# Performance work log

Hardware: AMD Instinct MI355X
Metric: run time of the kernel (lower is better)

The kernel has to match this reference:

```python
import jax, jax.numpy as jnp
import numpy as np

SEQ, BATCH = 64, 32
X_DIM, Z_DIM, Y_DIM, H_DIM, N_LAYERS = 32, 128, 16, 128, 3
PARAM_SHAPES = [(H_DIM, X_DIM), (H_DIM,), (H_DIM, H_DIM), (H_DIM,), (Y_DIM, H_DIM), (Y_DIM,)]
SIZES = [int(np.prod(s)) for s in PARAM_SHAPES]
NBLOCKS = [(s + Z_DIM - 1) // Z_DIM for s in SIZES]
OFFSETS = np.cumsum([0] + NBLOCKS)          # static block offsets per param tensor
TOTAL_NB = int(OFFSETS[-1])                  # 179 fastfood blocks total


def fwht(x):
    """Unnormalized Walsh-Hadamard transform over last axis (power-of-2 dim)."""
    d = x.shape[-1]
    h = 2
    while h <= d:
        x = x.reshape(x.shape[:-1] + (d // h, h))
        a, b = x[..., : h // 2], x[..., h // 2:]
        x = jnp.concatenate([a + b, a - b], axis=-1).reshape(x.shape[:-2] + (d,))
        h *= 2
    return x


def setup_inputs() -> dict:
    key = jax.random.key(0)
    ks = jax.random.split(key, 16)
    inp = {
        "x": jax.random.normal(ks[0], (SEQ, BATCH, X_DIM), jnp.float32),
        "z": jax.random.normal(ks[1], (SEQ, BATCH, Z_DIM), jnp.float32),
    }
    # base MLP parameters (nn.Linear default init: U(-1/sqrt(fan_in), 1/sqrt(fan_in)))
    for i in range(N_LAYERS):
        w_shape, b_shape = PARAM_SHAPES[2 * i], PARAM_SHAPES[2 * i + 1]
        s = 1.0 / np.sqrt(w_shape[1])
        inp[f"W0_{i}"] = jax.random.uniform(ks[2 + 2 * i], w_shape, jnp.float32, -s, s)
        inp[f"b0_{i}"] = jax.random.uniform(ks[3 + 2 * i], b_shape, jnp.float32, -s, s)
    # FastFood params stacked over all blocks of all param tensors
    inp["ffB"] = jnp.where(jax.random.bernoulli(ks[10], 0.5, (TOTAL_NB, Z_DIM)), 1.0, -1.0).astype(jnp.float32)
    inp["ffG"] = jax.random.normal(ks[11], (TOTAL_NB, Z_DIM), jnp.float32)
    inp["ffS"] = jax.random.normal(ks[12], (TOTAL_NB, Z_DIM), jnp.float32) * 0.01
    inp["ffP"] = jnp.argsort(jax.random.uniform(ks[13], (TOTAL_NB, Z_DIM)), axis=-1).astype(jnp.int32)
    return inp


def reference(x, z, W0_0, b0_0, W0_1, b0_1, W0_2, b0_2, ffB, ffG, ffS, ffP):
    N = SEQ * BATCH
    zf = z.reshape(N, Z_DIM)
    # FastFood upsample for all blocks at once: S * H * G * Pi * H * B * z
    v = ffB[None] * zf[:, None, :]                       # (N, NB, d)
    v = fwht(v)
    rows = jnp.arange(TOTAL_NB)[:, None]
    v = v[:, rows, ffP]                                  # per-block permutation
    v = ffG[None] * v
    v = fwht(v)
    v = ffS[None] * v / Z_DIM                            # (N, NB, d)

    Ws, bs = [W0_0, W0_1, W0_2], [b0_0, b0_1, b0_2]
    h = x
    for i in range(N_LAYERS):
        wi, bi = 2 * i, 2 * i + 1
        wd = v[:, OFFSETS[wi]:OFFSETS[wi + 1], :].reshape(N, -1)[:, :SIZES[wi]]
        wd = wd.reshape(SEQ, BATCH, *PARAM_SHAPES[wi])
        bd = v[:, OFFSETS[bi]:OFFSETS[bi + 1], :].reshape(N, -1)[:, :SIZES[bi]]
        bd = bd.reshape(SEQ, BATCH, *PARAM_SHAPES[bi])
        w = Ws[i][None, None] + wd                       # (seq, batch, out, in)
        b = bs[i][None, None] + bd                       # (seq, batch, out)
        h = jnp.einsum('sbi,sbji->sbj', h, w) + b
        if i < N_LAYERS - 1:
            h = jax.nn.relu(h)
    return h
```

## Files before the change

### kernel.cpp

```cpp
#include <hip/hip_runtime.h>
#include <hip/hip_fp16.h>


#define NTOK 2048

typedef _Float16 f16x8 __attribute__((ext_vector_type(8)));
typedef _Float16 f16x4 __attribute__((ext_vector_type(4)));
typedef float f32x4 __attribute__((ext_vector_type(4)));
typedef unsigned int u32;

__device__ __forceinline__ float2 pk_add(float2 a, float2 b) {
  float2 d;
  asm("v_pk_add_f32 %0, %1, %2" : "=v"(d) : "v"(a), "v"(b));
  return d;
}
__device__ __forceinline__ float2 pk_sub(float2 a, float2 b) {
  float2 d;
  asm("v_pk_add_f32 %0, %1, %2 neg_lo:[0,1] neg_hi:[0,1]" : "=v"(d) : "v"(a), "v"(b));
  return d;
}

__device__ __forceinline__ void fwht128p(float2 w[64]) {
#pragma unroll
  for (int m = 0; m < 64; m++) {
    float a = w[m].x, b = w[m].y;
    w[m].x = a + b; w[m].y = a - b;
  }
#pragma unroll
  for (int sig = 1; sig < 64; sig <<= 1) {
#pragma unroll
    for (int m = 0; m < 64; m++) {
      if ((m & sig) == 0) {
        float2 a = w[m], b = w[m + sig];
        w[m] = pk_add(a, b);
        w[m + sig] = pk_sub(a, b);
      }
    }
  }
}

__global__ __launch_bounds__(128) void km(
    const float* __restrict__ ffB, const float* __restrict__ ffG,
    const float* __restrict__ ffS, const int* __restrict__ ffP,
    _Float16* __restrict__ M) {
  __shared__ _Float16 T[128 * 128];
  __shared__ float sG[128], sS[128];
  __shared__ int sP[128];
  const int tid = threadIdx.x;
  const int j = blockIdx.x;
  sG[tid] = ffG[(size_t)j * 128 + tid];
  sS[tid] = ffS[(size_t)j * 128 + tid];
  sP[tid] = ffP[(size_t)j * 128 + tid];
  __syncthreads();
  const float Bc = ffB[(size_t)j * 128 + tid];
  float2 w[64];
#pragma unroll
  for (int m = 0; m < 64; m++) {
    int p0 = sP[2 * m], p1 = sP[2 * m + 1];
    float s0 = (__popc(p0 & tid) & 1) ? -Bc : Bc;
    float s1 = (__popc(p1 & tid) & 1) ? -Bc : Bc;
    w[m].x = sG[2 * m] * s0;
    w[m].y = sG[2 * m + 1] * s1;
  }
  fwht128p(w);
#pragma unroll
  for (int m = 0; m < 64; m++) {
    T[(2 * m) * 128 + tid] = (_Float16)(w[m].x * sS[2 * m] * 0.0078125f);
    T[(2 * m + 1) * 128 + tid] = (_Float16)(w[m].y * sS[2 * m + 1] * 0.0078125f);
  }
  __syncthreads();
  const u32* Ts = (const u32*)T;
  u32* Mo = (u32*)(M + (size_t)j * 16384);
#pragma unroll 4
  for (int i = 0; i < 64; i++) Mo[i * 128 + tid] = Ts[i * 128 + tid];
}

template <int MODE, int JB>
__global__ __launch_bounds__(256, 2) void gf(
    const _Float16* __restrict__ M, const float* __restrict__ z,
    int j0, int jbias,
    const float* __restrict__ xin,
    const float* __restrict__ hin,
    const float* __restrict__ Wp, const float* __restrict__ bp,
    float* __restrict__ outp) {
  __shared__ _Float16 Asm[128 * 136];
  __shared__ _Float16 Bsm[128 * 136];
  __shared__ _Float16 pM[4 * 136];
  __shared__ float pW[128];
  const int tid = threadIdx.x;
  const int lane = tid & 63, wv = tid >> 6;
  const int ln = lane & 15, g = lane >> 4;
  const int strip = blockIdx.x;
  const int tl0 = wv * 32 + ln;
  const int tg0 = strip * 128 + tl0;

  {
    const float4* zg = (const float4*)z + (size_t)(strip * 128) * 32;
#pragma unroll
    for (int i = 0; i < 16; i++) {
      int F = i * 256 + tid;
      int t = F >> 5, q = F & 31;
      float4 f = zg[(size_t)t * 32 + q];
      __half2 hlo = __floats2half2_rn(f.x, f.y);
      __half2 hhi = __floats2half2_rn(f.z, f.w);
      uint2 u = make_uint2(*(u32*)&hlo, *(u32*)&hhi);
      *(uint2*)(&Bsm[t * 136 + q * 4]) = u;
    }
  }

  float4 xa[2][2];
  if constexpr (MODE == 0) {
#pragma unroll
    for (int tt = 0; tt < 2; tt++) {
      const float* xr = xin + (size_t)(tg0 + tt * 16) * 32;
      xa[tt][0] = *(const float4*)(xr + g * 4);
      xa[tt][1] = *(const float4*)(xr + 16 + g * 4);
    }
  }

#pragma unroll 1
  for (int jj = 0; jj < JB; jj++) {
    const int row = blockIdx.y * JB + jj;
    const int j = j0 + row;

    {
      const uint4* Mg = (const uint4*)(M + (size_t)j * 16384);
#pragma unroll
      for (int i = 0; i < 8; i++) {
        int F = i * 256 + tid;
        int v = F >> 4, c = F & 15;
        *(uint4*)(&Asm[v * 136 + c * 8]) = Mg[F];
      }
    }
    if constexpr (MODE == 0) {
      {
        const u32* src = (const u32*)(M + (size_t)jbias * 16384 + (size_t)(4 * j) * 128);
        int rr = tid >> 6, uu = tid & 63;
        *(u32*)(&pM[rr * 136 + uu * 2]) = src[rr * 64 + uu];
      }
      if (tid < 128) pW[tid] = Wp[(size_t)(4 * j) * 32 + tid];
    } else {
      if (tid < 64) {
        const u32* src = (const u32*)(M + (size_t)jbias * 16384 + (size_t)row * 128);
        *(u32*)(&pM[tid * 2]) = src[tid];
      }
      if (tid < 128) pW[tid] = Wp[(size_t)row * 128 + tid];
    }
    __syncthreads();

    f32x4 acc[8][2];
#pragma unroll
    for (int vt = 0; vt < 8; vt++)
#pragma unroll
      for (int tt = 0; tt < 2; tt++) {
        f32x4 zf = {0.f, 0.f, 0.f, 0.f};
        acc[vt][tt] = zf;
      }
#pragma unroll
    for (int ks = 0; ks < 4; ks++) {
      f16x8 af[8], bf[2];
#pragma unroll
      for (int vt = 0; vt < 8; vt++)
        af[vt] = *(const f16x8*)(&Asm[(vt * 16 + ln) * 136 + ks * 32 + g * 8]);
#pragma unroll
      for (int tt = 0; tt < 2; tt++)
        bf[tt] = *(const f16x8*)(&Bsm[(wv * 32 + tt * 16 + ln) * 136 + ks * 32 + g * 8]);
#pragma unroll
      for (int vt = 0; vt < 8; vt++)
#pragma unroll
        for (int tt = 0; tt < 2; tt++)
          acc[vt][tt] = __builtin_amdgcn_mfma_f32_16x16x32_f16(af[vt], bf[tt],
                                                               acc[vt][tt], 0, 0, 0);
    }

    if constexpr (MODE == 0) {
      float pw[2][4] = {{0, 0, 0, 0}, {0, 0, 0, 0}};
      float pb[2][4] = {{0, 0, 0, 0}, {0, 0, 0, 0}};
#pragma unroll
      for (int vt = 0; vt < 8; vt++) {
        const int rho = vt >> 1;
        const float4 w4 = *(const float4*)&pW[rho * 32 + (vt & 1) * 16 + g * 4];
#pragma unroll
        for (int r = 0; r < 4; r++) {
          const float* xp0 = &xa[0][vt & 1].x;
          const float* xp1 = &xa[1][vt & 1].x;
          const float* wp4 = &w4.x;
          pw[0][rho] += acc[vt][0][r] * xp0[r];
          pw[1][rho] += acc[vt][1][r] * xp1[r];
          pb[0][rho] += wp4[r] * xp0[r];
          pb[1][rho] += wp4[r] * xp1[r];
        }
      }
#pragma unroll
      for (int tt = 0; tt < 2; tt++) {
#pragma unroll
        for (int uu = 0; uu < 8; uu++) {
          int u0 = g * 32 + uu * 4;
          f16x4 zh = *(const f16x4*)(&Bsm[(tl0 + tt * 16) * 136 + u0]);
          float zf0 = (float)zh[0], zf1 = (float)zh[1], zf2 = (float)zh[2], zf3 = (float)zh[3];
#pragma unroll
          for (int rho = 0; rho < 4; rho++) {
            f16x4 mh = *(const f16x4*)(&pM[rho * 136 + u0]);
            pw[tt][rho] += (float)mh[0] * zf0 + (float)mh[1] * zf1 +
                           (float)mh[2] * zf2 + (float)mh[3] * zf3;
          }
        }
      }
#pragma unroll
      for (int tt = 0; tt < 2; tt++)
#pragma unroll
        for (int rho = 0; rho < 4; rho++) {
          pw[tt][rho] += __shfl_xor(pw[tt][rho], 16);
          pw[tt][rho] += __shfl_xor(pw[tt][rho], 32);
          pb[tt][rho] += __shfl_xor(pb[tt][rho], 16);
          pb[tt][rho] += __shfl_xor(pb[tt][rho], 32);
        }
      if (g == 0) {
#pragma unroll
        for (int tt = 0; tt < 2; tt++) {
          float4 o;
          float* op = &o.x;
#pragma unroll
          for (int rho = 0; rho < 4; rho++)
            op[rho] = fmaxf(pb[tt][rho] + pw[tt][rho] + bp[4 * j + rho], 0.f);
          *(float4*)(outp + (size_t)(tg0 + tt * 16) * 128 + 4 * j) = o;
        }
      }
    } else {
      float pw0 = 0.f, pw1 = 0.f, pb0 = 0.f, pb1 = 0.f;
#pragma unroll
      for (int vt = 0; vt < 8; vt++) {
        const int v0 = vt * 16 + g * 4;
        const float4 w4 = *(const float4*)&pW[v0];
        const float4 h0 = *(const float4*)(hin + (size_t)tg0 * 128 + v0);
        const float4 h1v = *(const float4*)(hin + (size_t)(tg0 + 16) * 128 + v0);
        const float* wp4 = &w4.x;
        const float* hp0 = &h0.x;
        const float* hp1 = &h1v.x;
#pragma unroll
        for (int r = 0; r < 4; r++) {
          pw0 += acc[vt][0][r] * hp0[r];
          pw1 += acc[vt][1][r] * hp1[r];
          pb0 += wp4[r] * hp0[r];
          pb1 += wp4[r] * hp1[r];
        }
      }
#pragma unroll
      for (int uu = 0; uu < 8; uu++) {
        int u0 = g * 32 + uu * 4;
        f16x4 mh = *(const f16x4*)(&pM[u0]);
        f16x4 z0 = *(const f16x4*)(&Bsm[tl0 * 136 + u0]);
        f16x4 z1 = *(const f16x4*)(&Bsm[(tl0 + 16) * 136 + u0]);
#pragma unroll
        for (int e = 0; e < 4; e++) {
          pw0 += (float)mh[e] * (float)z0[e];
          pw1 += (float)mh[e] * (float)z1[e];
        }
      }
      pw0 += __shfl_xor(pw0, 16); pw0 += __shfl_xor(pw0, 32);
      pw1 += __shfl_xor(pw1, 16); pw1 += __shfl_xor(pw1, 32);
      pb0 += __shfl_xor(pb0, 16); pb0 += __shfl_xor(pb0, 32);
      pb1 += __shfl_xor(pb1, 16); pb1 += __shfl_xor(pb1, 32);
      if (g == 0) {
        float bias = bp[row];
        float v0 = pb0 + pw0 + bias;
        float v1 = pb1 + pw1 + bias;
        if constexpr (MODE == 1) {
          outp[(size_t)tg0 * 128 + row] = fmaxf(v0, 0.f);
          outp[(size_t)(tg0 + 16) * 128 + row] = fmaxf(v1, 0.f);
        } else {
          outp[(size_t)tg0 * 16 + row] = v0;
          outp[(size_t)(tg0 + 16) * 16 + row] = v1;
        }
      }
    }
    __syncthreads();
  }
}

extern "C" void kernel_launch(void* const* d_in, const int* in_sizes, int n_in,
                              void* d_out, int out_size, void* d_ws, size_t ws_size,
                              hipStream_t stream) {
  const float* x  = (const float*)d_in[0];
  const float* z  = (const float*)d_in[1];
  const float* W0 = (const float*)d_in[2];
  const float* b0 = (const float*)d_in[3];
  const float* W1 = (const float*)d_in[4];
  const float* b1 = (const float*)d_in[5];
  const float* W2 = (const float*)d_in[6];
  const float* b2 = (const float*)d_in[7];
  const float* fB = (const float*)d_in[8];
  const float* fG = (const float*)d_in[9];
  const float* fS = (const float*)d_in[10];
  const int*   fP = (const int*)d_in[11];
  float* out = (float*)d_out;
  (void)ws_size;

  char* p = (char*)d_ws;
  _Float16* Mbuf = (_Float16*)p; p += (size_t)179 * 16384 * 2;
  float* h1 = (float*)p;         p += (size_t)NTOK * 128 * 4;
  float* h2 = (float*)p;         p += (size_t)NTOK * 128 * 4;

  km<<<dim3(179), 128, 0, stream>>>(fB, fG, fS, fP, Mbuf);
  gf<0, 2><<<dim3(16, 16), 256, 0, stream>>>(Mbuf, z, 0, 32, x, nullptr, W0, b0, h1);
  gf<1, 2><<<dim3(16, 64), 256, 0, stream>>>(Mbuf, z, 33, 161, nullptr, h1, W1, b1, h2);
  gf<2, 2><<<dim3(16, 8), 256, 0, stream>>>(Mbuf, z, 162, 178, nullptr, h2, W2, b2, out);
}
```

Measured before the change: 126.1 us.

## Fuse fastfood and three layer kernels into one cooperative persistent kernel

```diff
diff --git a/kernel.cpp b/kernel.cpp
--- a/kernel.cpp
+++ b/kernel.cpp
@@ -1,13 +1,19 @@
 #include <hip/hip_runtime.h>
 #include <hip/hip_fp16.h>
+#include <hip/hip_cooperative_groups.h>
+
+namespace cg = cooperative_groups;
 
 
 #define NTOK 2048
 
 typedef _Float16 f16x8 __attribute__((ext_vector_type(8)));
-typedef _Float16 f16x4 __attribute__((ext_vector_type(4)));
 typedef float f32x4 __attribute__((ext_vector_type(4)));
 typedef unsigned int u32;
+
+struct ShM { _Float16 T[128 * 128]; float sG[128]; float sS[128]; int sP[128]; };
+struct ShG { _Float16 Asm[128 * 136]; _Float16 pM[4 * 136]; float pW[128]; };
+union Sh { ShM m; ShG g; };
 
 __device__ __forceinline__ float2 pk_add(float2 a, float2 b) {
   float2 d;
@@ -39,74 +45,68 @@
   }
 }
 
-__global__ __launch_bounds__(128) void km(
-    const float* __restrict__ ffB, const float* __restrict__ ffG,
-    const float* __restrict__ ffS, const int* __restrict__ ffP,
+__device__ __forceinline__ void km_body(ShM& m, int tid, int j,
+    const float* __restrict__ fB, const float* __restrict__ fG,
+    const float* __restrict__ fS, const int* __restrict__ fP,
     _Float16* __restrict__ M) {
-  __shared__ _Float16 T[128 * 128];
-  __shared__ float sG[128], sS[128];
-  __shared__ int sP[128];
-  const int tid = threadIdx.x;
-  const int j = blockIdx.x;
-  sG[tid] = ffG[(size_t)j * 128 + tid];
-  sS[tid] = ffS[(size_t)j * 128 + tid];
-  sP[tid] = ffP[(size_t)j * 128 + tid];
+  if (tid < 128) {
+    m.sG[tid] = fG[(size_t)j * 128 + tid];
+    m.sS[tid] = fS[(size_t)j * 128 + tid];
+    m.sP[tid] = fP[(size_t)j * 128 + tid];
+  }
   __syncthreads();
-  const float Bc = ffB[(size_t)j * 128 + tid];
-  float2 w[64];
-#pragma unroll
-  for (int m = 0; m < 64; m++) {
-    int p0 = sP[2 * m], p1 = sP[2 * m + 1];
-    float s0 = (__popc(p0 & tid) & 1) ? -Bc : Bc;
-    float s1 = (__popc(p1 & tid) & 1) ? -Bc : Bc;
-    w[m].x = sG[2 * m] * s0;
-    w[m].y = sG[2 * m + 1] * s1;
-  }
-  fwht128p(w);
-#pragma unroll
-  for (int m = 0; m < 64; m++) {
-    T[(2 * m) * 128 + tid] = (_Float16)(w[m].x * sS[2 * m] * 0.0078125f);
-    T[(2 * m + 1) * 128 + tid] = (_Float16)(w[m].y * sS[2 * m + 1] * 0.0078125f);
+  if (tid < 128) {
+    const float Bc = fB[(size_t)j * 128 + tid];
+    float2 w[64];
+#pragma unroll
+    for (int q = 0; q < 64; q++) {
+      int p0 = m.sP[2 * q], p1 = m.sP[2 * q + 1];
+      float s0 = (__popc(p0 & tid) & 1) ? -Bc : Bc;
+      float s1 = (__popc(p1 & tid) & 1) ? -Bc : Bc;
+      w[q].x = m.sG[2 * q] * s0;
+      w[q].y = m.sG[2 * q + 1] * s1;
+    }
+    fwht128p(w);
+#pragma unroll
+    for (int q = 0; q < 64; q++) {
+      m.T[(2 * q) * 128 + tid] = (_Float16)(w[q].x * m.sS[2 * q] * 0.0078125f);
+      m.T[(2 * q + 1) * 128 + tid] = (_Float16)(w[q].y * m.sS[2 * q + 1] * 0.0078125f);
+    }
   }
   __syncthreads();
-  const u32* Ts = (const u32*)T;
-  u32* Mo = (u32*)(M + (size_t)j * 16384);
+  if (tid < 128) {
+    const u32* Ts = (const u32*)m.T;
+    u32* Mo = (u32*)(M + (size_t)j * 16384);
 #pragma unroll 4
-  for (int i = 0; i < 64; i++) Mo[i * 128 + tid] = Ts[i * 128 + tid];
+    for (int i = 0; i < 64; i++) Mo[i * 128 + tid] = Ts[i * 128 + tid];
+  }
+}
+
+__device__ __forceinline__ void load_bf(f16x8 (&bf)[2][4],
+    const float* __restrict__ z, int tg0, int g) {
+#pragma unroll
+  for (int tt = 0; tt < 2; tt++)
+#pragma unroll
+    for (int ks = 0; ks < 4; ks++) {
+      const float* zp = z + (size_t)(tg0 + tt * 16) * 128 + ks * 32 + g * 8;
+      float4 a = *(const float4*)zp;
+      float4 b = *(const float4*)(zp + 4);
+      f16x8 v;
+      v[0] = (_Float16)a.x; v[1] = (_Float16)a.y; v[2] = (_Float16)a.z; v[3] = (_Float16)a.w;
+      v[4] = (_Float16)b.x; v[5] = (_Float16)b.y; v[6] = (_Float16)b.z; v[7] = (_Float16)b.w;
+      bf[tt][ks] = v;
+    }
 }
 
 template <int MODE, int JB>
-__global__ __launch_bounds__(256, 2) void gf(
-    const _Float16* __restrict__ M, const float* __restrict__ z,
-    int j0, int jbias,
-    const float* __restrict__ xin,
-    const float* __restrict__ hin,
+__device__ __forceinline__ void gf_phase(ShG& S, const f16x8 (&bf)[2][4],
+    const _Float16* __restrict__ M, int j0, int row0, int jbias,
+    const float* __restrict__ xin, const float* __restrict__ hin,
     const float* __restrict__ Wp, const float* __restrict__ bp,
-    float* __restrict__ outp) {
-  __shared__ _Float16 Asm[128 * 136];
-  __shared__ _Float16 Bsm[128 * 136];
-  __shared__ _Float16 pM[4 * 136];
-  __shared__ float pW[128];
-  const int tid = threadIdx.x;
+    float* __restrict__ outp, int tid, int strip) {
   const int lane = tid & 63, wv = tid >> 6;
   const int ln = lane & 15, g = lane >> 4;
-  const int strip = blockIdx.x;
-  const int tl0 = wv * 32 + ln;
-  const int tg0 = strip * 128 + tl0;
-
-  {
-    const float4* zg = (const float4*)z + (size_t)(strip * 128) * 32;
-#pragma unroll
-    for (int i = 0; i < 16; i++) {
-      int F = i * 256 + tid;
-      int t = F >> 5, q = F & 31;
-      float4 f = zg[(size_t)t * 32 + q];
-      __half2 hlo = __floats2half2_rn(f.x, f.y);
-      __half2 hhi = __floats2half2_rn(f.z, f.w);
-      uint2 u = make_uint2(*(u32*)&hlo, *(u32*)&hhi);
-      *(uint2*)(&Bsm[t * 136 + q * 4]) = u;
-    }
-  }
+  const int tg0 = strip * 128 + wv * 32 + ln;
 
   float4 xa[2][2];
   if constexpr (MODE == 0) {
@@ -120,31 +120,28 @@
 
 #pragma unroll 1
   for (int jj = 0; jj < JB; jj++) {
-    const int row = blockIdx.y * JB + jj;
-    const int j = j0 + row;
+    const int j = j0 + jj;
+    const int row = row0 + jj;
 
     {
       const uint4* Mg = (const uint4*)(M + (size_t)j * 16384);
 #pragma unroll
       for (int i = 0; i < 8; i++) {
         int F = i * 256 + tid;
-        int v = F >> 4, c = F & 15;
-        *(uint4*)(&Asm[v * 136 + c * 8]) = Mg[F];
+        *(uint4*)(&S.Asm[(F >> 4) * 136 + (F & 15) * 8]) = Mg[F];
       }
     }
     if constexpr (MODE == 0) {
-      {
-        const u32* src = (const u32*)(M + (size_t)jbias * 16384 + (size_t)(4 * j) * 128);
-        int rr = tid >> 6, uu = tid & 63;
-        *(u32*)(&pM[rr * 136 + uu * 2]) = src[rr * 64 + uu];
-      }
-      if (tid < 128) pW[tid] = Wp[(size_t)(4 * j) * 32 + tid];
+      const u32* src = (const u32*)(M + (size_t)jbias * 16384 + (size_t)(4 * j) * 128);
+      int rr = tid >> 6, uu = tid & 63;
+      *(u32*)(&S.pM[rr * 136 + uu * 2]) = src[rr * 64 + uu];
+      if (tid < 128) S.pW[tid] = Wp[(size_t)(4 * j) * 32 + tid];
     } else {
       if (tid < 64) {
         const u32* src = (const u32*)(M + (size_t)jbias * 16384 + (size_t)row * 128);
-        *(u32*)(&pM[tid * 2]) = src[tid];
-      }
-      if (tid < 128) pW[tid] = Wp[(size_t)row * 128 + tid];
+        *(u32*)(&S.pM[tid * 2]) = src[tid];
+      }
+      if (tid < 128) S.pW[tid] = Wp[(size_t)row * 128 + tid];
     }
     __syncthreads();
 
@@ -158,18 +155,15 @@
       }
 #pragma unroll
     for (int ks = 0; ks < 4; ks++) {
-      f16x8 af[8], bf[2];
+      f16x8 af[8];
 #pragma unroll
       for (int vt = 0; vt < 8; vt++)
-        af[vt] = *(const f16x8*)(&Asm[(vt * 16 + ln) * 136 + ks * 32 + g * 8]);
-#pragma unroll
-      for (int tt = 0; tt < 2; tt++)
-        bf[tt] = *(const f16x8*)(&Bsm[(wv * 32 + tt * 16 + ln) * 136 + ks * 32 + g * 8]);
+        af[vt] = *(const f16x8*)(&S.Asm[(vt * 16 + ln) * 136 + ks * 32 + g * 8]);
 #pragma unroll
       for (int vt = 0; vt < 8; vt++)
 #pragma unroll
         for (int tt = 0; tt < 2; tt++)
-          acc[vt][tt] = __builtin_amdgcn_mfma_f32_16x16x32_f16(af[vt], bf[tt],
+          acc[vt][tt] = __builtin_amdgcn_mfma_f32_16x16x32_f16(af[vt], bf[tt][ks],
                                                                acc[vt][tt], 0, 0, 0);
     }
 
@@ -179,7 +173,7 @@
 #pragma unroll
       for (int vt = 0; vt < 8; vt++) {
         const int rho = vt >> 1;
-        const float4 w4 = *(const float4*)&pW[rho * 32 + (vt & 1) * 16 + g * 4];
+        const float4 w4 = *(const float4*)&S.pW[rho * 32 + (vt & 1) * 16 + g * 4];
 #pragma unroll
         for (int r = 0; r < 4; r++) {
           const float* xp0 = &xa[0][vt & 1].x;
@@ -192,20 +186,18 @@
         }
       }
 #pragma unroll
-      for (int tt = 0; tt < 2; tt++) {
-#pragma unroll
-        for (int uu = 0; uu < 8; uu++) {
-          int u0 = g * 32 + uu * 4;
-          f16x4 zh = *(const f16x4*)(&Bsm[(tl0 + tt * 16) * 136 + u0]);
-          float zf0 = (float)zh[0], zf1 = (float)zh[1], zf2 = (float)zh[2], zf3 = (float)zh[3];
+      for (int tt = 0; tt < 2; tt++)
+#pragma unroll
+        for (int ks = 0; ks < 4; ks++) {
+          f16x8 zb = bf[tt][ks];
 #pragma unroll
           for (int rho = 0; rho < 4; rho++) {
-            f16x4 mh = *(const f16x4*)(&pM[rho * 136 + u0]);
-            pw[tt][rho] += (float)mh[0] * zf0 + (float)mh[1] * zf1 +
-                           (float)mh[2] * zf2 + (float)mh[3] * zf3;
+            f16x8 mh = *(const f16x8*)(&S.pM[rho * 136 + ks * 32 + g * 8]);
+#pragma unroll
+            for (int e = 0; e < 8; e++)
+              pw[tt][rho] += (float)mh[e] * (float)zb[e];
           }
         }
-      }
 #pragma unroll
       for (int tt = 0; tt < 2; tt++)
 #pragma unroll
@@ -231,7 +223,7 @@
 #pragma unroll
       for (int vt = 0; vt < 8; vt++) {
         const int v0 = vt * 16 + g * 4;
-        const float4 w4 = *(const float4*)&pW[v0];
+        const float4 w4 = *(const float4*)&S.pW[v0];
         const float4 h0 = *(const float4*)(hin + (size_t)tg0 * 128 + v0);
         const float4 h1v = *(const float4*)(hin + (size_t)(tg0 + 16) * 128 + v0);
         const float* wp4 = &w4.x;
@@ -246,13 +238,11 @@
         }
       }
 #pragma unroll
-      for (int uu = 0; uu < 8; uu++) {
-        int u0 = g * 32 + uu * 4;
-        f16x4 mh = *(const f16x4*)(&pM[u0]);
-        f16x4 z0 = *(const f16x4*)(&Bsm[tl0 * 136 + u0]);
-        f16x4 z1 = *(const f16x4*)(&Bsm[(tl0 + 16) * 136 + u0]);
-#pragma unroll
-        for (int e = 0; e < 4; e++) {
+      for (int ks = 0; ks < 4; ks++) {
+        f16x8 mh = *(const f16x8*)(&S.pM[ks * 32 + g * 8]);
+        f16x8 z0 = bf[0][ks], z1 = bf[1][ks];
+#pragma unroll
+        for (int e = 0; e < 8; e++) {
           pw0 += (float)mh[e] * (float)z0[e];
           pw1 += (float)mh[e] * (float)z1[e];
         }
@@ -276,6 +266,74 @@
     }
     __syncthreads();
   }
+}
+
+__global__ __launch_bounds__(256) void fused(
+    _Float16* __restrict__ M,
+    const float* __restrict__ z, const float* __restrict__ x,
+    const float* __restrict__ W0, const float* __restrict__ b0,
+    const float* __restrict__ W1, const float* __restrict__ b1,
+    const float* __restrict__ W2, const float* __restrict__ b2,
+    const float* __restrict__ fB, const float* __restrict__ fG,
+    const float* __restrict__ fS, const int* __restrict__ fP,
+    float* __restrict__ h1, float* __restrict__ h2, float* __restrict__ out) {
+  __shared__ Sh sh;
+  const int tid = threadIdx.x;
+  const int bid = blockIdx.x;
+  cg::grid_group grid = cg::this_grid();
+  const int strip = bid >> 4;
+  const int lane = tid & 63, wv = tid >> 6, ln = lane & 15, g = lane >> 4;
+  const int tg0 = strip * 128 + wv * 32 + ln;
+
+  f16x8 bf[2][4];
+  load_bf(bf, z, tg0, g);
+
+  if (bid < 179) km_body(sh.m, tid, bid, fB, fG, fS, fP, M);
+  __threadfence();
+  grid.sync();
+  __threadfence();
+
+  gf_phase<0, 2>(sh.g, bf, M, (bid & 15) * 2, (bid & 15) * 2, 32, x, nullptr,
+                 W0, b0, h1, tid, strip);
+  __threadfence();
+  grid.sync();
+  __threadfence();
+
+  gf_phase<1, 8>(sh.g, bf, M, 33 + (bid & 15) * 8, (bid & 15) * 8, 161, nullptr,
+                 h1, W1, b1, h2, tid, strip);
+  __threadfence();
+  grid.sync();
+  __threadfence();
+
+  gf_phase<2, 1>(sh.g, bf, M, 162 + (bid & 15), (bid & 15), 178, nullptr,
+                 h2, W2, b2, out, tid, strip);
+}
+
+__global__ __launch_bounds__(256) void km_k(
+    const float* __restrict__ fB, const float* __restrict__ fG,
+    const float* __restrict__ fS, const int* __restrict__ fP,
+    _Float16* __restrict__ M) {
+  __shared__ ShM m;
+  km_body(m, threadIdx.x, blockIdx.x, fB, fG, fS, fP, M);
+}
+
+template <int MODE, int JB>
+__global__ __launch_bounds__(256) void gf_k(
+    const _Float16* __restrict__ M, const float* __restrict__ z,
+    const float* __restrict__ xin, const float* __restrict__ hin,
+    const float* __restrict__ Wp, const float* __restrict__ bp,
+    float* __restrict__ outp) {
+  __shared__ ShG S;
+  const int tid = threadIdx.x;
+  const int strip = blockIdx.x;
+  const int lane = tid & 63, wv = tid >> 6, ln = lane & 15, g = lane >> 4;
+  const int tg0 = strip * 128 + wv * 32 + ln;
+  f16x8 bf[2][4];
+  load_bf(bf, z, tg0, g);
+  const int row0 = blockIdx.y * JB;
+  const int j0 = (MODE == 0) ? row0 : (MODE == 1 ? 33 + row0 : 162 + row0);
+  const int jbias = (MODE == 0) ? 32 : (MODE == 1 ? 161 : 178);
+  gf_phase<MODE, JB>(S, bf, M, j0, row0, jbias, xin, hin, Wp, bp, outp, tid, strip);
 }
 
 extern "C" void kernel_launch(void* const* d_in, const int* in_sizes, int n_in,
@@ -301,8 +359,14 @@
   float* h1 = (float*)p;         p += (size_t)NTOK * 128 * 4;
   float* h2 = (float*)p;         p += (size_t)NTOK * 128 * 4;
 
-  km<<<dim3(179), 128, 0, stream>>>(fB, fG, fS, fP, Mbuf);
-  gf<0, 2><<<dim3(16, 16), 256, 0, stream>>>(Mbuf, z, 0, 32, x, nullptr, W0, b0, h1);
-  gf<1, 2><<<dim3(16, 64), 256, 0, stream>>>(Mbuf, z, 33, 161, nullptr, h1, W1, b1, h2);
-  gf<2, 2><<<dim3(16, 8), 256, 0, stream>>>(Mbuf, z, 162, 178, nullptr, h2, W2, b2, out);
-}
+  void* args[] = {&Mbuf, &z, &x, &W0, &b0, &W1, &b1, &W2, &b2,
+                  &fB, &fG, &fS, &fP, &h1, &h2, &out};
+  hipError_t err = hipLaunchCooperativeKernel((const void*)fused, dim3(256),
+                                              dim3(256), args, 0, stream);
+  if (err != hipSuccess) {
+    km_k<<<dim3(179), 256, 0, stream>>>(fB, fG, fS, fP, Mbuf);
+    gf_k<0, 2><<<dim3(16, 16), 256, 0, stream>>>(Mbuf, z, x, nullptr, W0, b0, h1);
+    gf_k<1, 2><<<dim3(16, 64), 256, 0, stream>>>(Mbuf, z, nullptr, h1, W1, b1, h2);
+    gf_k<2, 2><<<dim3(16, 8), 256, 0, stream>>>(Mbuf, z, nullptr, h2, W2, b2, out);
+  }
+}
```

Result: slower. 380.7 us (+201.8%).

## Store M in MFMA fragment order and read operands directly from global memory

Applied to the files above, without the earlier changes.

```diff
diff --git a/kernel.cpp b/kernel.cpp
--- a/kernel.cpp
+++ b/kernel.cpp
@@ -5,7 +5,6 @@
 #define NTOK 2048
 
 typedef _Float16 f16x8 __attribute__((ext_vector_type(8)));
-typedef _Float16 f16x4 __attribute__((ext_vector_type(4)));
 typedef float f32x4 __attribute__((ext_vector_type(4)));
 typedef unsigned int u32;
 
@@ -40,73 +39,88 @@
 }
 
 __global__ __launch_bounds__(128) void km(
-    const float* __restrict__ ffB, const float* __restrict__ ffG,
-    const float* __restrict__ ffS, const int* __restrict__ ffP,
+    const float* __restrict__ fB, const float* __restrict__ fG,
+    const float* __restrict__ fS, const int* __restrict__ fP,
     _Float16* __restrict__ M) {
   __shared__ _Float16 T[128 * 128];
   __shared__ float sG[128], sS[128];
   __shared__ int sP[128];
   const int tid = threadIdx.x;
   const int j = blockIdx.x;
-  sG[tid] = ffG[(size_t)j * 128 + tid];
-  sS[tid] = ffS[(size_t)j * 128 + tid];
-  sP[tid] = ffP[(size_t)j * 128 + tid];
+  sG[tid] = fG[(size_t)j * 128 + tid];
+  sS[tid] = fS[(size_t)j * 128 + tid];
+  sP[tid] = fP[(size_t)j * 128 + tid];
   __syncthreads();
-  const float Bc = ffB[(size_t)j * 128 + tid];
+  const float Bc = fB[(size_t)j * 128 + tid];
   float2 w[64];
 #pragma unroll
-  for (int m = 0; m < 64; m++) {
-    int p0 = sP[2 * m], p1 = sP[2 * m + 1];
+  for (int q = 0; q < 64; q++) {
+    int p0 = sP[2 * q], p1 = sP[2 * q + 1];
     float s0 = (__popc(p0 & tid) & 1) ? -Bc : Bc;
     float s1 = (__popc(p1 & tid) & 1) ? -Bc : Bc;
-    w[m].x = sG[2 * m] * s0;
-    w[m].y = sG[2 * m + 1] * s1;
+    w[q].x = sG[2 * q] * s0;
+    w[q].y = sG[2 * q + 1] * s1;
   }
   fwht128p(w);
 #pragma unroll
-  for (int m = 0; m < 64; m++) {
-    T[(2 * m) * 128 + tid] = (_Float16)(w[m].x * sS[2 * m] * 0.0078125f);
-    T[(2 * m + 1) * 128 + tid] = (_Float16)(w[m].y * sS[2 * m + 1] * 0.0078125f);
+  for (int q = 0; q < 64; q++) {
+    T[(2 * q) * 128 + tid] = (_Float16)(w[q].x * sS[2 * q] * 0.0078125f);
+    T[(2 * q + 1) * 128 + tid] = (_Float16)(w[q].y * sS[2 * q + 1] * 0.0078125f);
   }
   __syncthreads();
   const u32* Ts = (const u32*)T;
   u32* Mo = (u32*)(M + (size_t)j * 16384);
-#pragma unroll 4
-  for (int i = 0; i < 64; i++) Mo[i * 128 + tid] = Ts[i * 128 + tid];
+#pragma unroll 8
+  for (int i = 0; i < 64; i++) {
+    int ww = i * 128 + tid;
+    int e2 = ww & 3, g = (ww >> 2) & 3, ln = (ww >> 4) & 15;
+    int ks = (ww >> 8) & 3, vt = ww >> 10;
+    Mo[ww] = Ts[(vt * 16 + ln) * 64 + ks * 16 + g * 4 + e2];
+  }
+}
+
+__device__ __forceinline__ void load_bf(f16x8 (&bf)[2][4],
+    const float* __restrict__ z, int tg0, int g) {
+#pragma unroll
+  for (int tt = 0; tt < 2; tt++)
+#pragma unroll
+    for (int ks = 0; ks < 4; ks++) {
+      const float* zp = z + (size_t)(tg0 + tt * 16) * 128 + ks * 32 + g * 8;
+      float4 a = *(const float4*)zp;
+      float4 b = *(const float4*)(zp + 4);
+      f16x8 v;
+      v[0] = (_Float16)a.x; v[1] = (_Float16)a.y; v[2] = (_Float16)a.z; v[3] = (_Float16)a.w;
+      v[4] = (_Float16)b.x; v[5] = (_Float16)b.y; v[6] = (_Float16)b.z; v[7] = (_Float16)b.w;
+      bf[tt][ks] = v;
+    }
+}
+
+__device__ __forceinline__ f16x8 ld_af(const _Float16* __restrict__ Aj,
+                                       int vt, int ks, int ln, int g) {
+  return *(const f16x8*)(Aj + ((size_t)((vt * 4 + ks) * 64 + ln * 4 + g)) * 8);
+}
+__device__ __forceinline__ f16x8 ld_mrow(const _Float16* __restrict__ Mb,
+                                         int rowv, int ks, int g) {
+  return *(const f16x8*)(Mb + ((size_t)(((rowv >> 4) * 4 + ks) * 64 +
+                                        (rowv & 15) * 4 + g)) * 8);
 }
 
 template <int MODE, int JB>
-__global__ __launch_bounds__(256, 2) void gf(
+__global__ __launch_bounds__(256) void gf_k(
     const _Float16* __restrict__ M, const float* __restrict__ z,
-    int j0, int jbias,
-    const float* __restrict__ xin,
-    const float* __restrict__ hin,
+    const float* __restrict__ xin, const float* __restrict__ hin,
     const float* __restrict__ Wp, const float* __restrict__ bp,
     float* __restrict__ outp) {
-  __shared__ _Float16 Asm[128 * 136];
-  __shared__ _Float16 Bsm[128 * 136];
-  __shared__ _Float16 pM[4 * 136];
-  __shared__ float pW[128];
   const int tid = threadIdx.x;
-  const int lane = tid & 63, wv = tid >> 6;
-  const int ln = lane & 15, g = lane >> 4;
   const int strip = blockIdx.x;
-  const int tl0 = wv * 32 + ln;
-  const int tg0 = strip * 128 + tl0;
-
-  {
-    const float4* zg = (const float4*)z + (size_t)(strip * 128) * 32;
-#pragma unroll
-    for (int i = 0; i < 16; i++) {
-      int F = i * 256 + tid;
-      int t = F >> 5, q = F & 31;
-      float4 f = zg[(size_t)t * 32 + q];
-      __half2 hlo = __floats2half2_rn(f.x, f.y);
-      __half2 hhi = __floats2half2_rn(f.z, f.w);
-      uint2 u = make_uint2(*(u32*)&hlo, *(u32*)&hhi);
-      *(uint2*)(&Bsm[t * 136 + q * 4]) = u;
-    }
-  }
+  const int lane = tid & 63, wv = tid >> 6, ln = lane & 15, g = lane >> 4;
+  const int tg0 = strip * 128 + wv * 32 + ln;
+  const int jbias = (MODE == 0) ? 32 : ((MODE == 1) ? 161 : 178);
+  const int j0 = ((MODE == 0) ? 0 : (MODE == 1) ? 33 : 162) + blockIdx.y * JB;
+  const _Float16* Mb = M + (size_t)jbias * 16384;
+
+  f16x8 bf[2][4];
+  load_bf(bf, z, tg0, g);
 
   float4 xa[2][2];
   if constexpr (MODE == 0) {
@@ -120,33 +134,9 @@
 
 #pragma unroll 1
   for (int jj = 0; jj < JB; jj++) {
-    const int row = blockIdx.y * JB + jj;
-    const int j = j0 + row;
-
-    {
-      const uint4* Mg = (const uint4*)(M + (size_t)j * 16384);
-#pragma unroll
-      for (int i = 0; i < 8; i++) {
-        int F = i * 256 + tid;
-        int v = F >> 4, c = F & 15;
-        *(uint4*)(&Asm[v * 136 + c * 8]) = Mg[F];
-      }
-    }
-    if constexpr (MODE == 0) {
-      {
-        const u32* src = (const u32*)(M + (size_t)jbias * 16384 + (size_t)(4 * j) * 128);
-        int rr = tid >> 6, uu = tid & 63;
-        *(u32*)(&pM[rr * 136 + uu * 2]) = src[rr * 64 + uu];
-      }
-      if (tid < 128) pW[tid] = Wp[(size_t)(4 * j) * 32 + tid];
-    } else {
-      if (tid < 64) {
-        const u32* src = (const u32*)(M + (size_t)jbias * 16384 + (size_t)row * 128);
-        *(u32*)(&pM[tid * 2]) = src[tid];
-      }
-      if (tid < 128) pW[tid] = Wp[(size_t)row * 128 + tid];
-    }
-    __syncthreads();
+    const int j = j0 + jj;
+    const int row = j - ((MODE == 0) ? 0 : (MODE == 1) ? 33 : 162);
+    const _Float16* Aj = M + (size_t)j * 16384;
 
     f32x4 acc[8][2];
 #pragma unroll
@@ -158,18 +148,14 @@
       }
 #pragma unroll
     for (int ks = 0; ks < 4; ks++) {
-      f16x8 af[8], bf[2];
+      f16x8 af[8];
+#pragma unroll
+      for (int vt = 0; vt < 8; vt++) af[vt] = ld_af(Aj, vt, ks, ln, g);
 #pragma unroll
       for (int vt = 0; vt < 8; vt++)
-        af[vt] = *(const f16x8*)(&Asm[(vt * 16 + ln) * 136 + ks * 32 + g * 8]);
-#pragma unroll
-      for (int tt = 0; tt < 2; tt++)
-        bf[tt] = *(const f16x8*)(&Bsm[(wv * 32 + tt * 16 + ln) * 136 + ks * 32 + g * 8]);
-#pragma unroll
-      for (int vt = 0; vt < 8; vt++)
 #pragma unroll
         for (int tt = 0; tt < 2; tt++)
-          acc[vt][tt] = __builtin_amdgcn_mfma_f32_16x16x32_f16(af[vt], bf[tt],
+          acc[vt][tt] = __builtin_amdgcn_mfma_f32_16x16x32_f16(af[vt], bf[tt][ks],
                                                                acc[vt][tt], 0, 0, 0);
     }
 
@@ -179,7 +165,8 @@
 #pragma unroll
       for (int vt = 0; vt < 8; vt++) {
         const int rho = vt >> 1;
-        const float4 w4 = *(const float4*)&pW[rho * 32 + (vt & 1) * 16 + g * 4];
+        const float4 w4 = *(const float4*)(Wp + (size_t)(4 * j + rho) * 32 +
+                                           (vt & 1) * 16 + g * 4);
 #pragma unroll
         for (int r = 0; r < 4; r++) {
           const float* xp0 = &xa[0][vt & 1].x;
@@ -192,17 +179,15 @@
         }
       }
 #pragma unroll
-      for (int tt = 0; tt < 2; tt++) {
-#pragma unroll
-        for (int uu = 0; uu < 8; uu++) {
-          int u0 = g * 32 + uu * 4;
-          f16x4 zh = *(const f16x4*)(&Bsm[(tl0 + tt * 16) * 136 + u0]);
-          float zf0 = (float)zh[0], zf1 = (float)zh[1], zf2 = (float)zh[2], zf3 = (float)zh[3];
-#pragma unroll
-          for (int rho = 0; rho < 4; rho++) {
-            f16x4 mh = *(const f16x4*)(&pM[rho * 136 + u0]);
-            pw[tt][rho] += (float)mh[0] * zf0 + (float)mh[1] * zf1 +
-                           (float)mh[2] * zf2 + (float)mh[3] * zf3;
+      for (int ks = 0; ks < 4; ks++) {
+        f16x8 zb0 = bf[0][ks], zb1 = bf[1][ks];
+#pragma unroll
+        for (int rho = 0; rho < 4; rho++) {
+          f16x8 mh = ld_mrow(Mb, 4 * j + rho, ks, g);
+#pragma unroll
+          for (int e = 0; e < 8; e++) {
+            pw[0][rho] += (float)mh[e] * (float)zb0[e];
+            pw[1][rho] += (float)mh[e] * (float)zb1[e];
           }
         }
       }
@@ -231,7 +216,7 @@
 #pragma unroll
       for (int vt = 0; vt < 8; vt++) {
         const int v0 = vt * 16 + g * 4;
-        const float4 w4 = *(const float4*)&pW[v0];
+        const float4 w4 = *(const float4*)(Wp + (size_t)row * 128 + v0);
         const float4 h0 = *(const float4*)(hin + (size_t)tg0 * 128 + v0);
         const float4 h1v = *(const float4*)(hin + (size_t)(tg0 + 16) * 128 + v0);
         const float* wp4 = &w4.x;
@@ -246,13 +231,11 @@
         }
       }
 #pragma unroll
-      for (int uu = 0; uu < 8; uu++) {
-        int u0 = g * 32 + uu * 4;
-        f16x4 mh = *(const f16x4*)(&pM[u0]);
-        f16x4 z0 = *(const f16x4*)(&Bsm[tl0 * 136 + u0]);
-        f16x4 z1 = *(const f16x4*)(&Bsm[(tl0 + 16) * 136 + u0]);
-#pragma unroll
-        for (int e = 0; e < 4; e++) {
+      for (int ks = 0; ks < 4; ks++) {
+        f16x8 mh = ld_mrow(Mb, row, ks, g);
+        f16x8 z0 = bf[0][ks], z1 = bf[1][ks];
+#pragma unroll
+        for (int e = 0; e < 8; e++) {
           pw0 += (float)mh[e] * (float)z0[e];
           pw1 += (float)mh[e] * (float)z1[e];
         }
@@ -274,7 +257,6 @@
         }
       }
     }
-    __syncthreads();
   }
 }
 
@@ -302,7 +284,7 @@
   float* h2 = (float*)p;         p += (size_t)NTOK * 128 * 4;
 
   km<<<dim3(179), 128, 0, stream>>>(fB, fG, fS, fP, Mbuf);
-  gf<0, 2><<<dim3(16, 16), 256, 0, stream>>>(Mbuf, z, 0, 32, x, nullptr, W0, b0, h1);
-  gf<1, 2><<<dim3(16, 64), 256, 0, stream>>>(Mbuf, z, 33, 161, nullptr, h1, W1, b1, h2);
-  gf<2, 2><<<dim3(16, 8), 256, 0, stream>>>(Mbuf, z, 162, 178, nullptr, h2, W2, b2, out);
-}
+  gf_k<0, 2><<<dim3(16, 16), 256, 0, stream>>>(Mbuf, z, x, nullptr, W0, b0, h1);
+  gf_k<1, 2><<<dim3(16, 64), 256, 0, stream>>>(Mbuf, z, nullptr, h1, W1, b1, h2);
+  gf_k<2, 2><<<dim3(16, 8), 256, 0, stream>>>(Mbuf, z, nullptr, h2, W2, b2, out);
+}
```

Measured after the change: 159.8 us. 26.7% more time.
